# Optimization experiments

Measured on AMD Instinct MI355X. Metric: run time of the kernel, lower is better.

The kernel has to match this reference:

```python
import jax, jax.numpy as jnp
import numpy as np

N, E, H = 50000, 800000, 128
EPS = 1e-5

def _init(key, shape, fan_in):
    return jax.random.normal(key, shape, dtype=jnp.float32) / np.sqrt(fan_in)

def setup_inputs() -> dict:
    key = jax.random.key(0)
    ks = jax.random.split(key, 20)
    x = jax.random.normal(ks[0], (N, 3), dtype=jnp.float32)
    h = jax.random.normal(ks[1], (N, H), dtype=jnp.float32)
    edge_index = jax.random.randint(ks[2], (2, E), 0, N, dtype=jnp.int32)
    d_ei = 2 * H + 1
    return {
        "x": x, "h": h, "edge_index": edge_index,
        "We1": _init(ks[3], (d_ei, H), d_ei), "be1": jnp.zeros((H,), jnp.float32),
        "We2": _init(ks[4], (H, H), H),       "be2": jnp.zeros((H,), jnp.float32),
        "Wc1": _init(ks[5], (H, H), H),       "bc1": jnp.zeros((H,), jnp.float32),
        "Wc2": _init(ks[6], (H, 1), H),       "bc2": jnp.zeros((1,), jnp.float32),
        "Wn1": _init(ks[7], (2 * H, H), 2 * H), "bn1": jnp.zeros((H,), jnp.float32),
        "Wn2": _init(ks[8], (H, H), H),       "bn2": jnp.zeros((H,), jnp.float32),
        "gamma": jnp.ones((H,), jnp.float32), "beta": jnp.zeros((H,), jnp.float32),
    }

def reference(x, h, edge_index, We1, be1, We2, be2, Wc1, bc1, Wc2, bc2,
              Wn1, bn1, Wn2, bn2, gamma, beta):
    act = jax.nn.silu
    row, col = edge_index[0], edge_index[1]
    n = x.shape[0]
    rel = x[row] - x[col]                                  # [E,3]
    dist2 = jnp.sum(rel * rel, axis=-1, keepdims=True)     # [E,1]
    edge_input = jnp.concatenate([h[row], h[col], dist2], axis=-1)  # [E,2H+1]
    ef = act(edge_input @ We1 + be1)
    ef = act(ef @ We2 + be2)                                # [E,H]
    gate = act(ef @ Wc1 + bc1) @ Wc2 + bc2                  # [E,1]
    # scatter-mean by row (shared counts for coords and features)
    counts = jax.ops.segment_sum(jnp.ones((rel.shape[0], 1), x.dtype), row, num_segments=n)
    counts = jnp.clip(counts, 1.0)
    dx = jax.ops.segment_sum(rel * gate, row, num_segments=n) / counts
    x_out = x + dx
    agg = jax.ops.segment_sum(ef, row, num_segments=n) / counts     # [N,H]
    dh = act(jnp.concatenate([h, agg], axis=-1) @ Wn1 + bn1) @ Wn2 + bn2
    h2 = h + dh
    mu = jnp.mean(h2, axis=-1, keepdims=True)
    var = jnp.mean((h2 - mu) ** 2, axis=-1, keepdims=True)
    h_norm = (h2 - mu) / jnp.sqrt(var + EPS) * gamma + beta
    h_out = act(h_norm)
    return x_out, h_out
```

## Files before the change

kernel.cpp:

```cpp
#include <hip/hip_runtime.h>

#define NN 50000
#define NE 800000
#define HD 128

typedef __attribute__((ext_vector_type(4))) float vf32x4;
typedef __attribute__((ext_vector_type(8))) __bf16 vbf16x8;
typedef __attribute__((ext_vector_type(4))) unsigned short vushort4;
typedef __attribute__((ext_vector_type(8))) unsigned short vushort8;

constexpr size_t OFF_AGG   = 0;
constexpr size_t OFF_DX    = 25600000;
constexpr size_t OFF_HIST  = 26200000;
constexpr size_t OFF_CUR   = 26400000;
constexpr size_t ZBYTES    = 26600000;
constexpr size_t OFF_START = 26600000;
constexpr size_t OFF_PERM  = 26800704;
constexpr size_t OFF_HBF   = 30000704;
constexpr size_t OFF_HR    = 42800704;
constexpr size_t OFF_HC    = 55600704;
constexpr size_t OFF_WE1P  = 68400704;
constexpr size_t OFF_WE2P  = OFF_WE1P + 65536;
constexpr size_t OFF_WC1P  = OFF_WE2P + 32768;
constexpr size_t OFF_WN1P  = OFF_WC1P + 32768;
constexpr size_t OFF_WN2P  = OFF_WN1P + 65536;
constexpr size_t OFF_BS    = OFF_WN2P + 32768;
constexpr size_t OFF_BO    = OFF_BS + 1024;

#define NB_SCAN 196

__device__ __forceinline__ unsigned short f2bf(float f) {
    unsigned int u = __float_as_uint(f);
    u += 0x7fffu + ((u >> 16) & 1u);
    return (unsigned short)(u >> 16);
}

__device__ __forceinline__ float bf2f(unsigned short b) {
    return __uint_as_float((unsigned int)b << 16);
}

__device__ __forceinline__ float silu(float v) {
    return __fdividef(v, 1.0f + __expf(-v));
}

__device__ __forceinline__ void pack_one(const float* __restrict__ src,
                                         unsigned short* __restrict__ dst,
                                         int local, int KB) {
    int j = local & 7;
    int lane = (local >> 3) & 63;
    int rest = local >> 9;
    int kb = rest % KB;
    int t = rest / KB;
    int srow = kb * 32 + ((lane >> 4) << 3) + j;
    int scol = t * 16 + (lane & 15);
    dst[local] = f2bf(src[srow * 128 + scol]);
}

__global__ __launch_bounds__(256) void pack_w_kernel(
    const float* __restrict__ We1, const float* __restrict__ We2,
    const float* __restrict__ Wc1, const float* __restrict__ Wn1,
    const float* __restrict__ Wn2,
    unsigned short* __restrict__ We1p, unsigned short* __restrict__ We2p,
    unsigned short* __restrict__ Wc1p, unsigned short* __restrict__ Wn1p,
    unsigned short* __restrict__ Wn2p) {
    int idx = blockIdx.x * 256 + threadIdx.x;
    if (idx < 32768)       pack_one(We1, We1p, idx, 8);
    else if (idx < 49152)  pack_one(We2, We2p, idx - 32768, 4);
    else if (idx < 65536)  pack_one(Wc1, Wc1p, idx - 49152, 4);
    else if (idx < 98304)  pack_one(Wn1, Wn1p, idx - 65536, 8);
    else                   pack_one(Wn2, Wn2p, idx - 98304, 4);
}

__global__ __launch_bounds__(256) void hist_kernel(const int* __restrict__ ei,
                                                   int* __restrict__ hist) {
    int e = blockIdx.x * 256 + threadIdx.x;
    atomicAdd(&hist[ei[e]], 1);
}

__global__ __launch_bounds__(256) void scanA_kernel(const int* __restrict__ hist,
                                                    int* __restrict__ blocksum) {
    __shared__ int sm[256];
    int i = blockIdx.x * 256 + threadIdx.x;
    sm[threadIdx.x] = (i < NN) ? hist[i] : 0;
    __syncthreads();
    for (int off = 128; off > 0; off >>= 1) {
        if (threadIdx.x < off) sm[threadIdx.x] += sm[threadIdx.x + off];
        __syncthreads();
    }
    if (threadIdx.x == 0) blocksum[blockIdx.x] = sm[0];
}

__global__ __launch_bounds__(256) void scanB_kernel(const int* __restrict__ blocksum,
                                                    int* __restrict__ blockoff) {
    __shared__ int sm[256];
    int t = threadIdx.x;
    int v = (t < NB_SCAN) ? blocksum[t] : 0;
    sm[t] = v;
    __syncthreads();
    for (int off = 1; off < 256; off <<= 1) {
        int u = (t >= off) ? sm[t - off] : 0;
        __syncthreads();
        sm[t] += u;
        __syncthreads();
    }
    if (t < NB_SCAN) blockoff[t] = sm[t] - v;
}

__global__ __launch_bounds__(256) void scanC_kernel(const int* __restrict__ hist,
                                                    const int* __restrict__ blockoff,
                                                    int* __restrict__ row_start) {
    __shared__ int sm[256];
    int i = blockIdx.x * 256 + threadIdx.x;
    int t = threadIdx.x;
    int v = (i < NN) ? hist[i] : 0;
    sm[t] = v;
    __syncthreads();
    for (int off = 1; off < 256; off <<= 1) {
        int u = (t >= off) ? sm[t - off] : 0;
        __syncthreads();
        sm[t] += u;
        __syncthreads();
    }
    if (i < NN) row_start[i] = blockoff[blockIdx.x] + sm[t] - v;
}

__global__ __launch_bounds__(256) void scatter_kernel(const int* __restrict__ ei,
                                                      const int* __restrict__ row_start,
                                                      int* __restrict__ cursor,
                                                      int* __restrict__ perm) {
    int e = blockIdx.x * 256 + threadIdx.x;
    int r = ei[e];
    int pos = row_start[r] + atomicAdd(&cursor[r], 1);
    perm[pos] = e;
}

__global__ __launch_bounds__(256, 4) void hprep_kernel(
    const float* __restrict__ h,
    const unsigned short* __restrict__ We1p,
    unsigned short* __restrict__ h_bf,
    unsigned short* __restrict__ hr, unsigned short* __restrict__ hc) {
    const int tid = threadIdx.x;
    const int nbase = blockIdx.x * 64;
    const int wave = tid >> 6, lane = tid & 63;
    const int li = lane & 15, grp = lane >> 4;

    int mynode = nbase + wave * 16 + li;
    if (mynode >= NN) mynode = NN - 1;

    vbf16x8 af[4];
    const float* ph = h + (size_t)mynode * 128 + grp * 8;
    unsigned short* pb = h_bf + (size_t)mynode * 128 + grp * 8;
#pragma unroll
    for (int kb = 0; kb < 4; kb++) {
        vf32x4 lo = *(const vf32x4*)(ph + kb * 32);
        vf32x4 hi = *(const vf32x4*)(ph + kb * 32 + 4);
        vushort8 o;
        o[0] = f2bf(lo[0]); o[1] = f2bf(lo[1]); o[2] = f2bf(lo[2]); o[3] = f2bf(lo[3]);
        o[4] = f2bf(hi[0]); o[5] = f2bf(hi[1]); o[6] = f2bf(hi[2]); o[7] = f2bf(hi[3]);
        *(vushort8*)(pb + kb * 32) = o;
        af[kb] = *(vbf16x8*)&o;
    }

    const vf32x4 vzero = {0.f, 0.f, 0.f, 0.f};
    vf32x4 ar[8], ac[8];
#pragma unroll
    for (int t = 0; t < 8; t++) { ar[t] = vzero; ac[t] = vzero; }
#pragma unroll
    for (int kb = 0; kb < 4; kb++) {
#pragma unroll
        for (int t = 0; t < 8; t++) {
            vbf16x8 br = *(const vbf16x8*)(We1p + ((t * 8 + kb) * 64 + lane) * 8);
            ar[t] = __builtin_amdgcn_mfma_f32_16x16x32_bf16(af[kb], br, ar[t], 0, 0, 0);
            vbf16x8 bc_ = *(const vbf16x8*)(We1p + ((t * 8 + 4 + kb) * 64 + lane) * 8);
            ac[t] = __builtin_amdgcn_mfma_f32_16x16x32_bf16(af[kb], bc_, ac[t], 0, 0, 0);
        }
    }
#pragma unroll
    for (int t = 0; t < 8; t++) {
        int col = t * 16 + li;
#pragma unroll
        for (int r = 0; r < 4; r++) {
            int node = nbase + wave * 16 + grp * 4 + r;
            if (node < NN) {
                hr[(size_t)node * 128 + col] = f2bf(ar[t][r]);
                hc[(size_t)node * 128 + col] = f2bf(ac[t][r]);
            }
        }
    }
}

__global__ __launch_bounds__(256, 8) void edge_kernel(
    const float* __restrict__ x, const int* __restrict__ ei,
    const int* __restrict__ perm,
    const unsigned short* __restrict__ hr, const unsigned short* __restrict__ hc,
    const unsigned short* __restrict__ We2p, const unsigned short* __restrict__ Wc1p,
    const float* __restrict__ We1, const float* __restrict__ be1,
    const float* __restrict__ be2, const float* __restrict__ bc1,
    const float* __restrict__ Wc2, const float* __restrict__ bc2,
    float* __restrict__ dxsum, float* __restrict__ agg) {

    __shared__ __align__(16) unsigned short s_ef[64 * 136];
    __shared__ float s_rel[64 * 4];
    __shared__ float s_wl[128];
    __shared__ float s_b1[128];
    __shared__ int s_row[64];
    __shared__ int s_col[64];

    const int tid = threadIdx.x;
    const int ebase = blockIdx.x * 64;

    if (tid < 64) {
        int e = perm[ebase + tid];
        int r = ei[e], c = ei[NE + e];
        s_row[tid] = r;
        s_col[tid] = c;
        float d0 = x[r * 3 + 0] - x[c * 3 + 0];
        float d1 = x[r * 3 + 1] - x[c * 3 + 1];
        float d2v = x[r * 3 + 2] - x[c * 3 + 2];
        s_rel[tid * 4 + 0] = d0;
        s_rel[tid * 4 + 1] = d1;
        s_rel[tid * 4 + 2] = d2v;
        s_rel[tid * 4 + 3] = d0 * d0 + d1 * d1 + d2v * d2v;
    }
    if (tid < 128) s_wl[tid] = We1[256 * 128 + tid];
    else           s_b1[tid - 128] = be1[tid - 128];
    __syncthreads();

    const int wave = tid >> 6, lane = tid & 63;
    const int li = lane & 15, grp = lane >> 4;
    const int el = wave * 16 + li;
    const vf32x4 vzero = {0.f, 0.f, 0.f, 0.f};

    vbf16x8 af[4];
    {
        const unsigned short* pr = hr + (size_t)s_row[el] * 128 + grp * 8;
        const unsigned short* pc = hc + (size_t)s_col[el] * 128 + grp * 8;
        const float d2e = s_rel[el * 4 + 3];
#pragma unroll
        for (int kb = 0; kb < 4; kb++) {
            vushort8 ua = *(const vushort8*)(pr + kb * 32);
            vushort8 ub = *(const vushort8*)(pc + kb * 32);
            int cbase = kb * 32 + grp * 8;
            vushort8 o;
#pragma unroll
            for (int j = 0; j < 8; j++) {
                float v = bf2f(ua[j]) + bf2f(ub[j]) + d2e * s_wl[cbase + j] + s_b1[cbase + j];
                o[j] = f2bf(silu(v));
            }
            af[kb] = *(vbf16x8*)&o;
        }
    }

    vf32x4 acc[8];
#pragma unroll
    for (int t = 0; t < 8; t++) acc[t] = vzero;
#pragma unroll
    for (int kb = 0; kb < 4; kb++) {
#pragma unroll
        for (int t = 0; t < 8; t++) {
            vbf16x8 b = *(const vbf16x8*)(We2p + ((t * 4 + kb) * 64 + lane) * 8);
            acc[t] = __builtin_amdgcn_mfma_f32_16x16x32_bf16(af[kb], b, acc[t], 0, 0, 0);
        }
    }
#pragma unroll
    for (int t = 0; t < 8; t++) {
        int col = t * 16 + li;
        float b2 = be2[col];
#pragma unroll
        for (int r = 0; r < 4; r++)
            s_ef[(wave * 16 + grp * 4 + r) * 136 + col] = f2bf(silu(acc[t][r] + b2));
    }
    __syncthreads();

#pragma unroll
    for (int t = 0; t < 8; t++) acc[t] = vzero;
    {
        const unsigned short* arow = s_ef + (wave * 16 + li) * 136 + grp * 8;
#pragma unroll
        for (int kb = 0; kb < 4; kb++) {
            vbf16x8 a = *(const vbf16x8*)(arow + kb * 32);
#pragma unroll
            for (int t = 0; t < 8; t++) {
                vbf16x8 b = *(const vbf16x8*)(Wc1p + ((t * 4 + kb) * 64 + lane) * 8);
                acc[t] = __builtin_amdgcn_mfma_f32_16x16x32_bf16(a, b, acc[t], 0, 0, 0);
            }
        }
    }
    float gp[4] = {0.f, 0.f, 0.f, 0.f};
#pragma unroll
    for (int t = 0; t < 8; t++) {
        int col = t * 16 + li;
        float bc = bc1[col], w2 = Wc2[col];
#pragma unroll
        for (int r = 0; r < 4; r++) gp[r] += silu(acc[t][r] + bc) * w2;
    }
#pragma unroll
    for (int r = 0; r < 4; r++) {
#pragma unroll
        for (int d = 1; d < 16; d <<= 1) gp[r] += __shfl_xor(gp[r], d, 16);
        gp[r] += bc2[0];
    }

#pragma unroll
    for (int r = 0; r < 4; r++) {
        int e2 = wave * 16 + grp * 4 + r;
        int node = s_row[e2];
        if (li < 3)
            atomicAdd(&dxsum[node * 3 + li], s_rel[e2 * 4 + li] * gp[r]);
    }

    {
        int p = tid & 63;
        int q = tid >> 6;
        int ebeg = q * 16;
        float a0 = 0.f, a1 = 0.f;
        int cur = s_row[ebeg];
#pragma unroll 4
        for (int e = ebeg; e < ebeg + 16; ++e) {
            int rr = s_row[e];
            unsigned int u = *(const unsigned int*)(s_ef + e * 136 + p * 2);
            float v0 = bf2f((unsigned short)(u & 0xffffu));
            float v1 = bf2f((unsigned short)(u >> 16));
            if (rr != cur) {
                atomicAdd(&agg[(size_t)cur * 128 + p * 2], a0);
                atomicAdd(&agg[(size_t)cur * 128 + p * 2 + 1], a1);
                a0 = 0.f; a1 = 0.f;
                cur = rr;
            }
            a0 += v0; a1 += v1;
        }
        atomicAdd(&agg[(size_t)cur * 128 + p * 2], a0);
        atomicAdd(&agg[(size_t)cur * 128 + p * 2 + 1], a1);
    }
}

__global__ __launch_bounds__(256, 4) void node_kernel(
    const float* __restrict__ x, const float* __restrict__ h32,
    const unsigned short* __restrict__ h_bf,
    const int* __restrict__ hist, const float* __restrict__ dxsum,
    const float* __restrict__ agg,
    const unsigned short* __restrict__ Wn1p, const unsigned short* __restrict__ Wn2p,
    const float* __restrict__ bn1, const float* __restrict__ bn2,
    const float* __restrict__ gamma, const float* __restrict__ beta,
    float* __restrict__ out) {

    __shared__ __align__(16) unsigned short s_agg[64 * 136];
    __shared__ __align__(16) unsigned short s_ef[64 * 136];

    const int tid = threadIdx.x;
    const int nbase = blockIdx.x * 64;

    {
        int idx = blockIdx.x * 192 + tid;
        if (tid < 192 && idx < NN * 3) {
            int node = idx / 3;
            float cnt = fmaxf((float)hist[node], 1.0f);
            out[idx] = x[idx] + dxsum[idx] / cnt;
        }
    }
#pragma unroll
    for (int i = 0; i < 8; i++) {
        int flat = i * 256 + tid;
        int row = flat >> 5, q = flat & 31;
        int node = nbase + row;
        if (node >= NN) node = NN - 1;
        float inv = 1.0f / fmaxf((float)hist[node], 1.0f);
        vf32x4 v = *(const vf32x4*)(agg + (size_t)node * 128 + q * 4);
        vushort4 o;
        o[0] = f2bf(v[0] * inv); o[1] = f2bf(v[1] * inv);
        o[2] = f2bf(v[2] * inv); o[3] = f2bf(v[3] * inv);
        *(vushort4*)(&s_agg[row * 136 + q * 4]) = o;
    }
    __syncthreads();

    const int wave = tid >> 6, lane = tid & 63;
    const int li = lane & 15, grp = lane >> 4;
    const vf32x4 vzero = {0.f, 0.f, 0.f, 0.f};

    int mynode = nbase + wave * 16 + li;
    if (mynode >= NN) mynode = NN - 1;

    vbf16x8 af[8];
    {
        const unsigned short* ph = h_bf + (size_t)mynode * 128 + grp * 8;
#pragma unroll
        for (int kb = 0; kb < 4; kb++) af[kb] = *(const vbf16x8*)(ph + kb * 32);
        const unsigned short* pa = s_agg + (wave * 16 + li) * 136 + grp * 8;
#pragma unroll
        for (int kb = 0; kb < 4; kb++) af[4 + kb] = *(const vbf16x8*)(pa + kb * 32);
    }
    vf32x4 acc[8];
#pragma unroll
    for (int t = 0; t < 8; t++) acc[t] = vzero;
#pragma unroll
    for (int kb = 0; kb < 8; kb++) {
#pragma unroll
        for (int t = 0; t < 8; t++) {
            vbf16x8 b = *(const vbf16x8*)(Wn1p + ((t * 8 + kb) * 64 + lane) * 8);
            acc[t] = __builtin_amdgcn_mfma_f32_16x16x32_bf16(af[kb], b, acc[t], 0, 0, 0);
        }
    }
#pragma unroll
    for (int t = 0; t < 8; t++) {
        int col = t * 16 + li;
        float b1 = bn1[col];
#pragma unroll
        for (int r = 0; r < 4; r++) {
            float v = silu(acc[t][r] + b1);
            s_ef[(wave * 16 + grp * 4 + r) * 136 + col] = f2bf(v);
        }
    }
    __syncthreads();

#pragma unroll
    for (int t = 0; t < 8; t++) acc[t] = vzero;
    {
        const unsigned short* arow = s_ef + (wave * 16 + li) * 136 + grp * 8;
#pragma unroll
        for (int kb = 0; kb < 4; kb++) {
            vbf16x8 a = *(const vbf16x8*)(arow + kb * 32);
#pragma unroll
            for (int t = 0; t < 8; t++) {
                vbf16x8 b = *(const vbf16x8*)(Wn2p + ((t * 4 + kb) * 64 + lane) * 8);
                acc[t] = __builtin_amdgcn_mfma_f32_16x16x32_bf16(a, b, acc[t], 0, 0, 0);
            }
        }
    }
    float h2v[8][4];
    float sum[4] = {0.f, 0.f, 0.f, 0.f}, sq[4] = {0.f, 0.f, 0.f, 0.f};
#pragma unroll
    for (int t = 0; t < 8; t++) {
        int col = t * 16 + li;
        float b2 = bn2[col];
#pragma unroll
        for (int r = 0; r < 4; r++) {
            int node = nbase + wave * 16 + grp * 4 + r;
            int nc = node < NN ? node : NN - 1;
            float v = acc[t][r] + b2 + h32[(size_t)nc * 128 + col];
            h2v[t][r] = v;
            sum[r] += v;
            sq[r] += v * v;
        }
    }
    float mu[4], rstd[4];
#pragma unroll
    for (int r = 0; r < 4; r++) {
#pragma unroll
        for (int d = 1; d < 16; d <<= 1) {
            sum[r] += __shfl_xor(sum[r], d, 16);
            sq[r] += __shfl_xor(sq[r], d, 16);
        }
        mu[r] = sum[r] * (1.0f / 128.0f);
        float var = sq[r] * (1.0f / 128.0f) - mu[r] * mu[r];
        rstd[r] = rsqrtf(var + 1e-5f);
    }
#pragma unroll
    for (int t = 0; t < 8; t++) {
        int col = t * 16 + li;
        float g = gamma[col], bt = beta[col];
#pragma unroll
        for (int r = 0; r < 4; r++) {
            int node = nbase + wave * 16 + grp * 4 + r;
            if (node < NN) {
                float vn = (h2v[t][r] - mu[r]) * rstd[r] * g + bt;
                out[NN * 3 + (size_t)node * 128 + col] = silu(vn);
            }
        }
    }
}

extern "C" void kernel_launch(void* const* d_in, const int* in_sizes, int n_in,
                              void* d_out, int out_size, void* d_ws, size_t ws_size,
                              hipStream_t stream) {
    const float* x     = (const float*)d_in[0];
    const float* h     = (const float*)d_in[1];
    const int* ei      = (const int*)d_in[2];
    const float* We1   = (const float*)d_in[3];
    const float* be1   = (const float*)d_in[4];
    const float* We2   = (const float*)d_in[5];
    const float* be2   = (const float*)d_in[6];
    const float* Wc1   = (const float*)d_in[7];
    const float* bc1   = (const float*)d_in[8];
    const float* Wc2   = (const float*)d_in[9];
    const float* bc2   = (const float*)d_in[10];
    const float* Wn1   = (const float*)d_in[11];
    const float* bn1   = (const float*)d_in[12];
    const float* Wn2   = (const float*)d_in[13];
    const float* bn2   = (const float*)d_in[14];
    const float* gamma = (const float*)d_in[15];
    const float* beta  = (const float*)d_in[16];
    float* out = (float*)d_out;

    char* ws = (char*)d_ws;
    float* agg            = (float*)(ws + OFF_AGG);
    float* dxsum          = (float*)(ws + OFF_DX);
    int* hist             = (int*)(ws + OFF_HIST);
    int* cursor           = (int*)(ws + OFF_CUR);
    int* row_start        = (int*)(ws + OFF_START);
    int* perm             = (int*)(ws + OFF_PERM);
    unsigned short* h_bf  = (unsigned short*)(ws + OFF_HBF);
    unsigned short* hr_bf = (unsigned short*)(ws + OFF_HR);
    unsigned short* hc_bf = (unsigned short*)(ws + OFF_HC);
    unsigned short* We1p  = (unsigned short*)(ws + OFF_WE1P);
    unsigned short* We2p  = (unsigned short*)(ws + OFF_WE2P);
    unsigned short* Wc1p  = (unsigned short*)(ws + OFF_WC1P);
    unsigned short* Wn1p  = (unsigned short*)(ws + OFF_WN1P);
    unsigned short* Wn2p  = (unsigned short*)(ws + OFF_WN2P);
    int* blocksum         = (int*)(ws + OFF_BS);
    int* blockoff         = (int*)(ws + OFF_BO);

    hipMemsetAsync(ws, 0, ZBYTES, stream);
    pack_w_kernel<<<114688 / 256, 256, 0, stream>>>(We1, We2, Wc1, Wn1, Wn2,
                                                    We1p, We2p, Wc1p, Wn1p, Wn2p);
    hist_kernel<<<NE / 256, 256, 0, stream>>>(ei, hist);
    scanA_kernel<<<NB_SCAN, 256, 0, stream>>>(hist, blocksum);
    scanB_kernel<<<1, 256, 0, stream>>>(blocksum, blockoff);
    scanC_kernel<<<NB_SCAN, 256, 0, stream>>>(hist, blockoff, row_start);
    scatter_kernel<<<NE / 256, 256, 0, stream>>>(ei, row_start, cursor, perm);
    hprep_kernel<<<(NN + 63) / 64, 256, 0, stream>>>(h, We1p, h_bf, hr_bf, hc_bf);
    edge_kernel<<<NE / 64, 256, 0, stream>>>(x, ei, perm, hr_bf, hc_bf, We2p, Wc1p,
                                             We1, be1, be2, bc1, Wc2, bc2,
                                             dxsum, agg);
    node_kernel<<<(NN + 63) / 64, 256, 0, stream>>>(x, h, h_bf, hist, dxsum, agg,
                                                    Wn1p, Wn2p, bn1, bn2, gamma, beta, out);
}
```

Measured before the change: 496.2 us.

## Merge pack+hist and scatter+hprep launches, fold be1 into hr, use native bf16 cast

```diff
diff --git a/kernel.cpp b/kernel.cpp
--- a/kernel.cpp
+++ b/kernel.cpp
@@ -28,11 +28,13 @@
 constexpr size_t OFF_BO    = OFF_BS + 1024;
 
 #define NB_SCAN 196
+#define NB_PACK 448
+#define NB_HIST 3125
+#define NB_HPREP 782
 
 __device__ __forceinline__ unsigned short f2bf(float f) {
-    unsigned int u = __float_as_uint(f);
-    u += 0x7fffu + ((u >> 16) & 1u);
-    return (unsigned short)(u >> 16);
+    __bf16 b = (__bf16)f;
+    return __builtin_bit_cast(unsigned short, b);
 }
 
 __device__ __forceinline__ float bf2f(unsigned short b) {
@@ -56,25 +58,26 @@
     dst[local] = f2bf(src[srow * 128 + scol]);
 }
 
-__global__ __launch_bounds__(256) void pack_w_kernel(
+__global__ __launch_bounds__(256) void pack_hist_kernel(
     const float* __restrict__ We1, const float* __restrict__ We2,
     const float* __restrict__ Wc1, const float* __restrict__ Wn1,
     const float* __restrict__ Wn2,
     unsigned short* __restrict__ We1p, unsigned short* __restrict__ We2p,
     unsigned short* __restrict__ Wc1p, unsigned short* __restrict__ Wn1p,
-    unsigned short* __restrict__ Wn2p) {
-    int idx = blockIdx.x * 256 + threadIdx.x;
-    if (idx < 32768)       pack_one(We1, We1p, idx, 8);
-    else if (idx < 49152)  pack_one(We2, We2p, idx - 32768, 4);
-    else if (idx < 65536)  pack_one(Wc1, Wc1p, idx - 49152, 4);
-    else if (idx < 98304)  pack_one(Wn1, Wn1p, idx - 65536, 8);
-    else                   pack_one(Wn2, Wn2p, idx - 98304, 4);
-}
-
-__global__ __launch_bounds__(256) void hist_kernel(const int* __restrict__ ei,
-                                                   int* __restrict__ hist) {
-    int e = blockIdx.x * 256 + threadIdx.x;
-    atomicAdd(&hist[ei[e]], 1);
+    unsigned short* __restrict__ Wn2p,
+    const int* __restrict__ ei, int* __restrict__ hist) {
+    int b = blockIdx.x;
+    if (b < NB_PACK) {
+        int idx = b * 256 + threadIdx.x;
+        if (idx < 32768)       pack_one(We1, We1p, idx, 8);
+        else if (idx < 49152)  pack_one(We2, We2p, idx - 32768, 4);
+        else if (idx < 65536)  pack_one(Wc1, Wc1p, idx - 49152, 4);
+        else if (idx < 98304)  pack_one(Wn1, Wn1p, idx - 65536, 8);
+        else                   pack_one(Wn2, Wn2p, idx - 98304, 4);
+    } else {
+        int e = (b - NB_PACK) * 256 + threadIdx.x;
+        atomicAdd(&hist[ei[e]], 1);
+    }
 }
 
 __global__ __launch_bounds__(256) void scanA_kernel(const int* __restrict__ hist,
@@ -124,23 +127,24 @@
     if (i < NN) row_start[i] = blockoff[blockIdx.x] + sm[t] - v;
 }
 
-__global__ __launch_bounds__(256) void scatter_kernel(const int* __restrict__ ei,
-                                                      const int* __restrict__ row_start,
-                                                      int* __restrict__ cursor,
-                                                      int* __restrict__ perm) {
-    int e = blockIdx.x * 256 + threadIdx.x;
-    int r = ei[e];
-    int pos = row_start[r] + atomicAdd(&cursor[r], 1);
-    perm[pos] = e;
-}
-
-__global__ __launch_bounds__(256, 4) void hprep_kernel(
-    const float* __restrict__ h,
-    const unsigned short* __restrict__ We1p,
+__global__ __launch_bounds__(256, 4) void scatter_hprep_kernel(
+    const int* __restrict__ ei, const int* __restrict__ row_start,
+    int* __restrict__ cursor, int* __restrict__ perm,
+    const float* __restrict__ h, const unsigned short* __restrict__ We1p,
+    const float* __restrict__ be1,
     unsigned short* __restrict__ h_bf,
     unsigned short* __restrict__ hr, unsigned short* __restrict__ hc) {
+
+    if (blockIdx.x < NB_HIST) {
+        int e = blockIdx.x * 256 + threadIdx.x;
+        int r = ei[e];
+        int pos = row_start[r] + atomicAdd(&cursor[r], 1);
+        perm[pos] = e;
+        return;
+    }
+
     const int tid = threadIdx.x;
-    const int nbase = blockIdx.x * 64;
+    const int nbase = (blockIdx.x - NB_HIST) * 64;
     const int wave = tid >> 6, lane = tid & 63;
     const int li = lane & 15, grp = lane >> 4;
 
@@ -178,11 +182,12 @@
 #pragma unroll
     for (int t = 0; t < 8; t++) {
         int col = t * 16 + li;
+        float b1 = be1[col];
 #pragma unroll
         for (int r = 0; r < 4; r++) {
             int node = nbase + wave * 16 + grp * 4 + r;
             if (node < NN) {
-                hr[(size_t)node * 128 + col] = f2bf(ar[t][r]);
+                hr[(size_t)node * 128 + col] = f2bf(ar[t][r] + b1);
                 hc[(size_t)node * 128 + col] = f2bf(ac[t][r]);
             }
         }
@@ -194,7 +199,7 @@
     const int* __restrict__ perm,
     const unsigned short* __restrict__ hr, const unsigned short* __restrict__ hc,
     const unsigned short* __restrict__ We2p, const unsigned short* __restrict__ Wc1p,
-    const float* __restrict__ We1, const float* __restrict__ be1,
+    const float* __restrict__ We1,
     const float* __restrict__ be2, const float* __restrict__ bc1,
     const float* __restrict__ Wc2, const float* __restrict__ bc2,
     float* __restrict__ dxsum, float* __restrict__ agg) {
@@ -202,7 +207,6 @@
     __shared__ __align__(16) unsigned short s_ef[64 * 136];
     __shared__ float s_rel[64 * 4];
     __shared__ float s_wl[128];
-    __shared__ float s_b1[128];
     __shared__ int s_row[64];
     __shared__ int s_col[64];
 
@@ -222,8 +226,7 @@
         s_rel[tid * 4 + 2] = d2v;
         s_rel[tid * 4 + 3] = d0 * d0 + d1 * d1 + d2v * d2v;
     }
-    if (tid < 128) s_wl[tid] = We1[256 * 128 + tid];
-    else           s_b1[tid - 128] = be1[tid - 128];
+    if (tid >= 128 && tid < 256) s_wl[tid - 128] = We1[256 * 128 + (tid - 128)];
     __syncthreads();
 
     const int wave = tid >> 6, lane = tid & 63;
@@ -240,14 +243,14 @@
         for (int kb = 0; kb < 4; kb++) {
             vushort8 ua = *(const vushort8*)(pr + kb * 32);
             vushort8 ub = *(const vushort8*)(pc + kb * 32);
-            int cbase = kb * 32 + grp * 8;
-            vushort8 o;
+            const float* wl = s_wl + kb * 32 + grp * 8;
+            vbf16x8 o;
 #pragma unroll
             for (int j = 0; j < 8; j++) {
-                float v = bf2f(ua[j]) + bf2f(ub[j]) + d2e * s_wl[cbase + j] + s_b1[cbase + j];
-                o[j] = f2bf(silu(v));
+                float v = bf2f(ua[j]) + bf2f(ub[j]) + d2e * wl[j];
+                o[j] = (__bf16)silu(v);
             }
-            af[kb] = *(vbf16x8*)&o;
+            af[kb] = o;
         }
     }
 
@@ -510,16 +513,15 @@
     int* blockoff         = (int*)(ws + OFF_BO);
 
     hipMemsetAsync(ws, 0, ZBYTES, stream);
-    pack_w_kernel<<<114688 / 256, 256, 0, stream>>>(We1, We2, Wc1, Wn1, Wn2,
-                                                    We1p, We2p, Wc1p, Wn1p, Wn2p);
-    hist_kernel<<<NE / 256, 256, 0, stream>>>(ei, hist);
+    pack_hist_kernel<<<NB_PACK + NB_HIST, 256, 0, stream>>>(
+        We1, We2, Wc1, Wn1, Wn2, We1p, We2p, Wc1p, Wn1p, Wn2p, ei, hist);
     scanA_kernel<<<NB_SCAN, 256, 0, stream>>>(hist, blocksum);
     scanB_kernel<<<1, 256, 0, stream>>>(blocksum, blockoff);
     scanC_kernel<<<NB_SCAN, 256, 0, stream>>>(hist, blockoff, row_start);
-    scatter_kernel<<<NE / 256, 256, 0, stream>>>(ei, row_start, cursor, perm);
-    hprep_kernel<<<(NN + 63) / 64, 256, 0, stream>>>(h, We1p, h_bf, hr_bf, hc_bf);
+    scatter_hprep_kernel<<<NB_HIST + NB_HPREP, 256, 0, stream>>>(
+        ei, row_start, cursor, perm, h, We1p, be1, h_bf, hr_bf, hc_bf);
     edge_kernel<<<NE / 64, 256, 0, stream>>>(x, ei, perm, hr_bf, hc_bf, We2p, Wc1p,
-                                             We1, be1, be2, bc1, Wc2, bc2,
+                                             We1, be2, bc1, Wc2, bc2,
                                              dxsum, agg);
     node_kernel<<<(NN + 63) / 64, 256, 0, stream>>>(x, h, h_bf, hist, dxsum, agg,
                                                     Wn1p, Wn2p, bn1, bn2, gamma, beta, out);
```

Measured after the change: 501.5 us, median of 2. Within noise of the previous version (+1.1%).
